# Kernel optimization log

Measured on AMD Instinct MI355X. Metric: run time of the kernel, lower is better.

Reference implementation:

```python
import jax, jax.numpy as jnp
import numpy as np

B, S, D, E2 = 64, 512, 1024, 1024  # batch, enc seq len, dec hidden, 2*enc hidden


def setup_inputs() -> dict:
    key = jax.random.key(0)
    ks = jax.random.split(key, 5)
    scale = 1.0 / np.sqrt(D + E2)
    return {
        "dec_state": jax.random.normal(ks[0], (B, D), jnp.float32),
        "enc_states": jax.random.normal(ks[1], (B, S, E2), jnp.float32),
        "att_mask": jnp.ones((B, S), jnp.int32),
        "w_weight": jax.random.normal(ks[2], (D, D + E2), jnp.float32) * scale,
        "w_bias": jax.random.normal(ks[3], (D,), jnp.float32) * scale,
        "v_weight": jax.random.normal(ks[4], (D,), jnp.float32) * (1.0 / np.sqrt(D)),
    }


def reference(dec_state, enc_states, att_mask, w_weight, w_bias, v_weight):
    # Additive (Bahdanau) attention. Split the concat-linear into two GEMMs:
    # tanh(W [dec; enc] + b) == tanh(dec @ Wd^T + enc @ We^T + b) -- same math,
    # avoids materializing the repeated/concatenated [B,S,D+2E] tensor.
    Wd = w_weight[:, :dec_state.shape[-1]]          # [D, D]
    We = w_weight[:, dec_state.shape[-1]:]          # [D, 2E]
    dec_proj = jnp.einsum('bd,kd->bk', dec_state, Wd)        # [B, D]
    enc_proj = jnp.einsum('bse,ke->bsk', enc_states, We)     # [B, S, D]
    energy = jnp.tanh(enc_proj + dec_proj[:, None, :] + w_bias)  # [B, S, D]
    attention = jnp.einsum('bsk,k->bs', energy, v_weight)    # [B, S]
    attention = jnp.where(att_mask == 0, -jnp.inf, attention)
    att_weights = jax.nn.softmax(attention, axis=1)          # [B, S]
    att_out = jnp.einsum('bs,bse->be', att_weights, enc_states)[:, None, :]  # [B,1,2E]
    return att_out
```

## Files before the change

### kernel.cpp

```cpp
#include <hip/hip_runtime.h>
#include <hip/hip_bf16.h>
#include <math.h>

#define B_  64
#define S_  512
#define D_  1024
#define E2_ 1024
#define WROW (D_ + E2_)
#define NTILES 4

typedef __attribute__((ext_vector_type(8))) short bf16x8;
typedef __attribute__((ext_vector_type(4))) float f32x4;
typedef __attribute__((ext_vector_type(8))) unsigned short u16x8;

__device__ __forceinline__ unsigned short f2bf(float f) {
    unsigned u = __float_as_uint(f);
    u = (u + 0x7FFFu + ((u >> 16) & 1u)) >> 16;
    return (unsigned short)u;
}

__device__ __forceinline__ float bf2f(unsigned short u) {
    return __uint_as_float((unsigned)u << 16);
}

__device__ __forceinline__ void load_lds16(const void* g, void* l) {
    __builtin_amdgcn_global_load_lds(
        (__attribute__((address_space(1))) void*)(void*)g,
        (__attribute__((address_space(3))) void*)l,
        16, 0, 0);
}

__device__ __forceinline__ float fast_tanh(float x) {
    float ax = fminf(fabsf(x), 16.0f);
    float t  = __builtin_amdgcn_exp2f(ax * 2.8853900817779268f);
    float r  = (t - 1.0f) * __builtin_amdgcn_rcpf(t + 1.0f);
    return copysignf(r, x);
}

__global__ __launch_bounds__(256) void conv_enc_kernel(
        const float* __restrict__ in, unsigned short* __restrict__ out, int n8)
{
    int i = blockIdx.x * 256 + threadIdx.x;
    const int stride = gridDim.x * 256;
    for (; i < n8; i += stride) {
        float4 a = *reinterpret_cast<const float4*>(in + (size_t)i * 8);
        float4 b = *reinterpret_cast<const float4*>(in + (size_t)i * 8 + 4);
        u16x8 o;
        o[0] = f2bf(a.x); o[1] = f2bf(a.y); o[2] = f2bf(a.z); o[3] = f2bf(a.w);
        o[4] = f2bf(b.x); o[5] = f2bf(b.y); o[6] = f2bf(b.z); o[7] = f2bf(b.w);
        *reinterpret_cast<u16x8*>(out + (size_t)i * 8) = o;
    }
}

__global__ __launch_bounds__(256) void conv_we_kernel(
        const float* __restrict__ w, unsigned short* __restrict__ web)
{
    const int k = blockIdx.x;
    const int j = threadIdx.x * 4;
    float4 a = *reinterpret_cast<const float4*>(w + (size_t)k * WROW + D_ + j);
    ushort4 o;
    o.x = f2bf(a.x); o.y = f2bf(a.y); o.z = f2bf(a.z); o.w = f2bf(a.w);
    *reinterpret_cast<ushort4*>(web + (size_t)k * E2_ + j) = o;
}

__global__ __launch_bounds__(256) void dec_proj_kernel(
        const float* __restrict__ dec,
        const float* __restrict__ w,
        const float* __restrict__ bias,
        float* __restrict__ t)
{
    __shared__ float wrow[D_];
    __shared__ float red[256];
    const int k = blockIdx.x;
    const int tid = threadIdx.x;

    const float* wr = w + (size_t)k * WROW;
    for (int i = tid; i < D_; i += 256) wrow[i] = wr[i];
    __syncthreads();

    const int b = tid >> 2;
    const int q = tid & 3;
    const float* dp = dec + b * D_ + q * 256;
    const float* wp = wrow + q * 256;
    float acc = 0.f;
    #pragma unroll 8
    for (int i = 0; i < 256; ++i) acc = fmaf(dp[i], wp[i], acc);
    red[tid] = acc;
    __syncthreads();
    if (q == 0) {
        float s = red[tid] + red[tid + 1] + red[tid + 2] + red[tid + 3];
        t[b * D_ + k] = s + bias[k];
    }
}

#define BME 256
#define BNE 256
#define BKE 64
#define KT_ (E2_ / BKE)

__global__ __launch_bounds__(512, 2) void energy_mfma_kernel(
        const unsigned short* __restrict__ encb,
        const unsigned short* __restrict__ web,
        const float* __restrict__ t,
        const float* __restrict__ v,
        float* __restrict__ att_part)
{
    __shared__ __align__(16) unsigned short As[2][BME * BKE];
    __shared__ __align__(16) unsigned short Bs[2][BNE * BKE];
    __shared__ float tv_s[BNE];
    __shared__ float vv_s[BNE];
    __shared__ float red[4][BME];

    const int g     = blockIdx.x;
    const int mblk  = (g & 7) + 8 * (g >> 5);
    const int ntile = (g >> 3) & 3;

    const int m0 = mblk * BME;
    const int n0 = ntile * BNE;
    const int b  = m0 >> 9;
    const int tid = threadIdx.x;
    const int w   = tid >> 6;
    const int l   = tid & 63;
    const int wm  = w >> 2;
    const int wn  = w & 3;

    if (tid < BNE) {
        tv_s[tid] = t[b * D_ + n0 + tid];
        vv_s[tid] = v[n0 + tid];
    }

    const int lr8 = l >> 3;
    const int lk  = 8 * ((l & 7) ^ lr8);
    const unsigned short* gA = encb + (size_t)m0 * E2_;
    const unsigned short* gB = web  + (size_t)n0 * E2_;

    const int rA = wm * 128 + (l & 15);
    const int rB = wn * 64 + (l & 15);
    const int kswz = (l & 7) << 4;
    const int khi  = (l >> 4) << 4;

    f32x4 acc[8][4] = {};

    auto stage = [&](int bf, int kt) {
        const int k0 = kt * BKE;
        #pragma unroll
        for (int r = 0; r < 4; ++r) {
            const int c = r * 8 + w;
            const int row = c * 8 + lr8;
            load_lds16(gA + (size_t)row * E2_ + k0 + lk,
                       (char*)As[bf] + c * 1024);
            load_lds16(gB + (size_t)row * E2_ + k0 + lk,
                       (char*)Bs[bf] + c * 1024);
        }
    };

    stage(0, 0);
    stage(1, 1);

    for (int kt = 0; kt < KT_; ++kt) {
        const int cur = kt & 1;
        if (kt + 1 < KT_) {
            asm volatile("s_waitcnt vmcnt(8)" ::: "memory");
        } else {
            asm volatile("s_waitcnt vmcnt(0)" ::: "memory");
        }
        __builtin_amdgcn_sched_barrier(0);
        __builtin_amdgcn_s_barrier();
        __builtin_amdgcn_sched_barrier(0);

        #pragma unroll
        for (int kk = 0; kk < 2; ++kk) {
            const int kb = (kk * 64 + khi) ^ kswz;
            bf16x8 a[8], bb[4];
            #pragma unroll
            for (int mi = 0; mi < 8; ++mi)
                a[mi] = *reinterpret_cast<const bf16x8*>(
                    (const char*)As[cur] + (rA + mi * 16) * 128 + kb);
            #pragma unroll
            for (int ni = 0; ni < 4; ++ni)
                bb[ni] = *reinterpret_cast<const bf16x8*>(
                    (const char*)Bs[cur] + (rB + ni * 16) * 128 + kb);
            __builtin_amdgcn_s_setprio(1);
            #pragma unroll
            for (int mi = 0; mi < 8; ++mi)
                #pragma unroll
                for (int ni = 0; ni < 4; ++ni)
                    acc[mi][ni] = __builtin_amdgcn_mfma_f32_16x16x32_bf16(
                        a[mi], bb[ni], acc[mi][ni], 0, 0, 0);
            __builtin_amdgcn_s_setprio(0);
        }

        __builtin_amdgcn_sched_barrier(0);
        __builtin_amdgcn_s_barrier();
        __builtin_amdgcn_sched_barrier(0);
        if (kt + 2 < KT_) stage(cur, kt + 2);
    }

    #pragma unroll
    for (int mi = 0; mi < 8; ++mi) {
        float P[4] = {0.f, 0.f, 0.f, 0.f};
        #pragma unroll
        for (int ni = 0; ni < 4; ++ni) {
            const int nl = wn * 64 + ni * 16 + (l & 15);
            const float tvv = tv_s[nl];
            const float vvv = vv_s[nl];
            #pragma unroll
            for (int j = 0; j < 4; ++j) {
                float e = fast_tanh(acc[mi][ni][j] + tvv);
                P[j] = fmaf(e, vvv, P[j]);
            }
        }
        #pragma unroll
        for (int j = 0; j < 4; ++j) {
            float p = P[j];
            p += __shfl_xor(p, 1);
            p += __shfl_xor(p, 2);
            p += __shfl_xor(p, 4);
            p += __shfl_xor(p, 8);
            if ((l & 15) == 0)
                red[wn][wm * 128 + mi * 16 + (l >> 4) * 4 + j] = p;
        }
    }
    __syncthreads();
    if (tid < BME)
        att_part[(size_t)(m0 + tid) * NTILES + ntile] =
            (red[0][tid] + red[1][tid]) + (red[2][tid] + red[3][tid]);
}

__global__ __launch_bounds__(256) void softmax_kernel(
        const float* __restrict__ att_part,
        const int* __restrict__ mask,
        float* __restrict__ wout)
{
    __shared__ float red[256];
    const int b = blockIdx.x;
    const int tid = threadIdx.x;

    float x0 = 0.f, x1 = 0.f;
    #pragma unroll
    for (int p = 0; p < NTILES; ++p) {
        x0 += att_part[(size_t)(b * S_ + tid) * NTILES + p];
        x1 += att_part[(size_t)(b * S_ + 256 + tid) * NTILES + p];
    }
    bool m0v = (mask[b * S_ + tid] != 0);
    bool m1v = (mask[b * S_ + 256 + tid] != 0);
    if (!m0v) x0 = -INFINITY;
    if (!m1v) x1 = -INFINITY;

    float m = fmaxf(x0, x1);
    red[tid] = m;
    __syncthreads();
    for (int o = 128; o > 0; o >>= 1) {
        if (tid < o) red[tid] = fmaxf(red[tid], red[tid + o]);
        __syncthreads();
    }
    m = red[0];
    __syncthreads();

    float e0 = m0v ? expf(x0 - m) : 0.f;
    float e1 = m1v ? expf(x1 - m) : 0.f;
    red[tid] = e0 + e1;
    __syncthreads();
    for (int o = 128; o > 0; o >>= 1) {
        if (tid < o) red[tid] += red[tid + o];
        __syncthreads();
    }
    const float inv = 1.f / red[0];
    wout[b * S_ + tid] = e0 * inv;
    wout[b * S_ + 256 + tid] = e1 * inv;
}

__global__ __launch_bounds__(128) void attout_part_kernel(
        const float* __restrict__ wgt,
        const unsigned short* __restrict__ encb,
        float* __restrict__ out_part)
{
    __shared__ float wsm[64];
    const int b  = blockIdx.y;
    const int sc = blockIdx.x;
    const int tid = threadIdx.x;
    if (tid < 64) wsm[tid] = wgt[b * S_ + sc * 64 + tid];
    __syncthreads();

    const unsigned short* ep =
        encb + ((size_t)b * S_ + sc * 64) * E2_ + tid * 8;
    float acc[8] = {};
    #pragma unroll 4
    for (int s = 0; s < 64; ++s) {
        u16x8 e8 = *reinterpret_cast<const u16x8*>(ep + (size_t)s * E2_);
        const float ws = wsm[s];
        #pragma unroll
        for (int j = 0; j < 8; ++j)
            acc[j] = fmaf(ws, bf2f((unsigned short)e8[j]), acc[j]);
    }
    float* op = out_part + ((size_t)sc * B_ + b) * E2_ + tid * 8;
    #pragma unroll
    for (int j = 0; j < 8; ++j) op[j] = acc[j];
}

__global__ __launch_bounds__(256) void attout_reduce_kernel(
        const float* __restrict__ out_part,
        float* __restrict__ out)
{
    const int idx = blockIdx.x * 256 + threadIdx.x;
    const int n4 = (B_ * E2_) / 4;
    const float4* p = reinterpret_cast<const float4*>(out_part);
    float4 r = p[idx];
    #pragma unroll
    for (int c = 1; c < 8; ++c) {
        float4 q = p[idx + c * n4];
        r.x += q.x; r.y += q.y; r.z += q.z; r.w += q.w;
    }
    reinterpret_cast<float4*>(out)[idx] = r;
}

extern "C" void kernel_launch(void* const* d_in, const int* in_sizes, int n_in,
                              void* d_out, int out_size, void* d_ws, size_t ws_size,
                              hipStream_t stream) {
    const float* dec  = (const float*)d_in[0];
    const float* enc  = (const float*)d_in[1];
    const int*   mask = (const int*)d_in[2];
    const float* w    = (const float*)d_in[3];
    const float* bias = (const float*)d_in[4];
    const float* v    = (const float*)d_in[5];
    float* out = (float*)d_out;

    float* t_buf    = (float*)d_ws;
    float* att_part = t_buf + B_ * D_;
    float* wgt_buf  = att_part + B_ * S_ * NTILES;
    float* out_part = wgt_buf + B_ * S_;
    unsigned short* encb = (unsigned short*)(out_part + 8 * B_ * E2_);
    unsigned short* web  = encb + (size_t)B_ * S_ * E2_;

    const int enc_n8 = (B_ * S_ * E2_) / 8;
    conv_enc_kernel<<<4096, 256, 0, stream>>>(enc, encb, enc_n8);
    conv_we_kernel<<<D_, 256, 0, stream>>>(w, web);
    dec_proj_kernel<<<D_, 256, 0, stream>>>(dec, w, bias, t_buf);
    energy_mfma_kernel<<<512, 512, 0, stream>>>(encb, web, t_buf, v, att_part);
    softmax_kernel<<<B_, 256, 0, stream>>>(att_part, mask, wgt_buf);
    attout_part_kernel<<<dim3(8, B_), 128, 0, stream>>>(wgt_buf, encb, out_part);
    attout_reduce_kernel<<<(B_ * E2_ / 4) / 256, 256, 0, stream>>>(out_part, out);
}
```

Measured before the change: 159.7 us.

## Split energy GEMM LDS staging into k-halves with finer-grained interleaved prefetch

Restructures the energy MFMA kernel's shared-memory pipeline. Each 64-wide K tile is now stored as two 32-wide halves with a new XOR swizzle. Global-to-LDS loads for the next tile are issued in small A and B pieces between MFMA sub-phases, replacing the earlier scheme that prefetched two whole tiles ahead. The aim is to spread memory traffic across the compute and cut register pressure from fragment loads. In exchange there are more barriers per K step, and prefetch runs only one tile ahead, which may expose latency.

```diff
diff --git a/kernel.cpp b/kernel.cpp
--- a/kernel.cpp
+++ b/kernel.cpp
@@ -105,8 +105,8 @@
         const float* __restrict__ v,
         float* __restrict__ att_part)
 {
-    __shared__ __align__(16) unsigned short As[2][BME * BKE];
-    __shared__ __align__(16) unsigned short Bs[2][BNE * BKE];
+    __shared__ __align__(16) unsigned short As[2][2][256 * 32];
+    __shared__ __align__(16) unsigned short Bs[2][2][256 * 32];
     __shared__ float tv_s[BNE];
     __shared__ float vv_s[BNE];
     __shared__ float red[4][BME];
@@ -129,71 +129,96 @@
         vv_s[tid] = v[n0 + tid];
     }
 
-    const int lr8 = l >> 3;
-    const int lk  = 8 * ((l & 7) ^ lr8);
+    const int srow = l >> 2;
+    const int scol = ((l & 3) ^ ((l >> 2) & 3)) * 8;
     const unsigned short* gA = encb + (size_t)m0 * E2_;
     const unsigned short* gB = web  + (size_t)n0 * E2_;
 
     const int rA = wm * 128 + (l & 15);
     const int rB = wn * 64 + (l & 15);
-    const int kswz = (l & 7) << 4;
-    const int khi  = (l >> 4) << 4;
+    const int fcol = (((l >> 4) << 4) ^ ((l & 3) << 4));
 
     f32x4 acc[8][4] = {};
 
-    auto stage = [&](int bf, int kt) {
-        const int k0 = kt * BKE;
-        #pragma unroll
-        for (int r = 0; r < 4; ++r) {
-            const int c = r * 8 + w;
-            const int row = c * 8 + lr8;
-            load_lds16(gA + (size_t)row * E2_ + k0 + lk,
-                       (char*)As[bf] + c * 1024);
-            load_lds16(gB + (size_t)row * E2_ + k0 + lk,
-                       (char*)Bs[bf] + c * 1024);
+    auto stageA = [&](int bf, int kt, int kk) {
+        const int kbase = kt * BKE + kk * 32;
+        #pragma unroll
+        for (int i = 0; i < 2; ++i) {
+            const int c = w * 2 + i;
+            const int row = c * 16 + srow;
+            load_lds16(gA + (size_t)row * E2_ + kbase + scol,
+                       (char*)&As[bf][kk][0] + c * 1024);
         }
     };
-
-    stage(0, 0);
-    stage(1, 1);
+    auto stageB = [&](int bf, int kt, int kk) {
+        const int kbase = kt * BKE + kk * 32;
+        #pragma unroll
+        for (int i = 0; i < 2; ++i) {
+            const int c = w * 2 + i;
+            const int row = c * 16 + srow;
+            load_lds16(gB + (size_t)row * E2_ + kbase + scol,
+                       (char*)&Bs[bf][kk][0] + c * 1024);
+        }
+    };
+
+    stageA(0, 0, 0); stageB(0, 0, 0); stageA(0, 0, 1); stageB(0, 0, 1);
+    asm volatile("s_waitcnt vmcnt(4)" ::: "memory");
+    __builtin_amdgcn_s_barrier();
+    __builtin_amdgcn_sched_barrier(0);
 
     for (int kt = 0; kt < KT_; ++kt) {
         const int cur = kt & 1;
-        if (kt + 1 < KT_) {
-            asm volatile("s_waitcnt vmcnt(8)" ::: "memory");
-        } else {
-            asm volatile("s_waitcnt vmcnt(0)" ::: "memory");
-        }
-        __builtin_amdgcn_sched_barrier(0);
-        __builtin_amdgcn_s_barrier();
-        __builtin_amdgcn_sched_barrier(0);
+        const int nxt = cur ^ 1;
+        const bool pre = (kt + 1 < KT_);
+        bf16x8 a[8], bb[2];
 
         #pragma unroll
         for (int kk = 0; kk < 2; ++kk) {
-            const int kb = (kk * 64 + khi) ^ kswz;
-            bf16x8 a[8], bb[4];
             #pragma unroll
             for (int mi = 0; mi < 8; ++mi)
                 a[mi] = *reinterpret_cast<const bf16x8*>(
-                    (const char*)As[cur] + (rA + mi * 16) * 128 + kb);
-            #pragma unroll
-            for (int ni = 0; ni < 4; ++ni)
-                bb[ni] = *reinterpret_cast<const bf16x8*>(
-                    (const char*)Bs[cur] + (rB + ni * 16) * 128 + kb);
+                    (const char*)&As[cur][kk][0] + (rA + mi * 16) * 64 + fcol);
+            #pragma unroll
+            for (int nj = 0; nj < 2; ++nj)
+                bb[nj] = *reinterpret_cast<const bf16x8*>(
+                    (const char*)&Bs[cur][kk][0] + (rB + nj * 16) * 64 + fcol);
+            if (pre) stageA(nxt, kt + 1, kk);
             __builtin_amdgcn_s_setprio(1);
             #pragma unroll
-            for (int mi = 0; mi < 8; ++mi)
-                #pragma unroll
-                for (int ni = 0; ni < 4; ++ni)
-                    acc[mi][ni] = __builtin_amdgcn_mfma_f32_16x16x32_bf16(
-                        a[mi], bb[ni], acc[mi][ni], 0, 0, 0);
+            for (int mi = 0; mi < 8; ++mi) {
+                acc[mi][0] = __builtin_amdgcn_mfma_f32_16x16x32_bf16(
+                    a[mi], bb[0], acc[mi][0], 0, 0, 0);
+                acc[mi][1] = __builtin_amdgcn_mfma_f32_16x16x32_bf16(
+                    a[mi], bb[1], acc[mi][1], 0, 0, 0);
+            }
             __builtin_amdgcn_s_setprio(0);
-        }
-
-        __builtin_amdgcn_sched_barrier(0);
-        __builtin_amdgcn_s_barrier();
-        __builtin_amdgcn_sched_barrier(0);
-        if (kt + 2 < KT_) stage(cur, kt + 2);
+            __builtin_amdgcn_sched_barrier(0);
+            __builtin_amdgcn_s_barrier();
+            __builtin_amdgcn_sched_barrier(0);
+
+            #pragma unroll
+            for (int nj = 0; nj < 2; ++nj)
+                bb[nj] = *reinterpret_cast<const bf16x8*>(
+                    (const char*)&Bs[cur][kk][0] + (rB + (2 + nj) * 16) * 64 + fcol);
+            if (pre) stageB(nxt, kt + 1, kk);
+            __builtin_amdgcn_s_setprio(1);
+            #pragma unroll
+            for (int mi = 0; mi < 8; ++mi) {
+                acc[mi][2] = __builtin_amdgcn_mfma_f32_16x16x32_bf16(
+                    a[mi], bb[0], acc[mi][2], 0, 0, 0);
+                acc[mi][3] = __builtin_amdgcn_mfma_f32_16x16x32_bf16(
+                    a[mi], bb[1], acc[mi][3], 0, 0, 0);
+            }
+            __builtin_amdgcn_s_setprio(0);
+            if (pre) {
+                asm volatile("s_waitcnt vmcnt(4)" ::: "memory");
+            } else if (kk == 0) {
+                asm volatile("s_waitcnt vmcnt(0)" ::: "memory");
+            }
+            __builtin_amdgcn_sched_barrier(0);
+            __builtin_amdgcn_s_barrier();
+            __builtin_amdgcn_sched_barrier(0);
+        }
     }
 
     #pragma unroll
```

After: 158.6 us. Within noise of the previous version (-0.7%).
